# Optimization experiments

Measured on AMD Instinct MI355X. Metric: run time of the kernel, lower is better.

Reference implementation:

```python
import jax, jax.numpy as jnp
import numpy as np

D_MODEL = 1024
NUM_HEADS = 16
D_K = D_MODEL // NUM_HEADS
R = 8
ALPHA = 16
SCALING = ALPHA / R


def _lora_linear(x, W, b, A, Bm):
    # base: x @ W.T + b ; lora: (x @ A.T) @ Bm.T * scaling
    base = jnp.einsum('btd,od->bto', x, W) + b
    lora = jnp.einsum('btr,or->bto', jnp.einsum('btd,rd->btr', x, A), Bm) * SCALING
    return base + lora


def setup_inputs() -> dict:
    key = jax.random.key(0)
    ks = jax.random.split(key, 20)
    B, T = 2, 2048
    inp = {
        'q': jax.random.normal(ks[0], (B, T, D_MODEL), jnp.float32),
        'k': jax.random.normal(ks[1], (B, T, D_MODEL), jnp.float32),
        'v': jax.random.normal(ks[2], (B, T, D_MODEL), jnp.float32),
        'mask': jnp.ones((1, 1, T, T), jnp.int32),
    }
    i = 3
    for name in ('q', 'k', 'v'):
        inp[f'W{name}'] = jax.random.normal(ks[i], (D_MODEL, D_MODEL), jnp.float32) * 0.02; i += 1
        inp[f'b{name}'] = jnp.zeros((D_MODEL,), jnp.float32)
        inp[f'A{name}'] = jax.random.normal(ks[i], (R, D_MODEL), jnp.float32) * 0.01; i += 1
        inp[f'B{name}'] = jax.random.normal(ks[i], (D_MODEL, R), jnp.float32) * 0.01; i += 1
    inp['Wo'] = jax.random.normal(ks[i], (D_MODEL, D_MODEL), jnp.float32) * 0.02
    inp['bo'] = jnp.zeros((D_MODEL,), jnp.float32)
    return inp


def reference(q, k, v, mask, Wq, bq, Aq, Bq, Wk, bk, Ak, Bk, Wv, bv, Av, Bv, Wo, bo):
    B, Tq, _ = q.shape
    Tk = k.shape[1]
    Q = _lora_linear(q, Wq, bq, Aq, Bq).reshape(B, Tq, NUM_HEADS, D_K).transpose(0, 2, 1, 3)
    K = _lora_linear(k, Wk, bk, Ak, Bk).reshape(B, Tk, NUM_HEADS, D_K).transpose(0, 2, 1, 3)
    V = _lora_linear(v, Wv, bv, Av, Bv).reshape(B, Tk, NUM_HEADS, D_K).transpose(0, 2, 1, 3)
    scores = jnp.einsum('bhqd,bhkd->bhqk', Q, K) / jnp.sqrt(jnp.float32(D_K))
    scores = jnp.where(mask == 0, jnp.float32(-1e9), scores)
    attn = jax.nn.softmax(scores, axis=-1)
    out = jnp.einsum('bhqk,bhkd->bhqd', attn, V)
    out = out.transpose(0, 2, 1, 3).reshape(B, Tq, D_MODEL)
    return jnp.einsum('btd,od->bto', out, Wo) + bo
```

## Files before the change

kernel.cpp:

```cpp
#include <hip/hip_runtime.h>
#include <stdint.h>

typedef unsigned short u16;
typedef __attribute__((ext_vector_type(4))) float f32x4;
typedef __attribute__((ext_vector_type(4))) uint32_t u32x4;
typedef __attribute__((ext_vector_type(8))) __bf16 bf16x8;

#if __has_builtin(__builtin_amdgcn_exp2f)
#define EXP2(x) __builtin_amdgcn_exp2f(x)
#else
#define EXP2(x) exp2f(x)
#endif

static __device__ __forceinline__ u16 f2bf(float f) {
    union { float f; uint32_t i; } v; v.f = f;
    return (u16)((v.i + 0x7FFFu + ((v.i >> 16) & 1u)) >> 16);
}
static __device__ __forceinline__ uint32_t cvtpk(float lo, float hi) {
    uint32_t r;
    asm("v_cvt_pk_bf16_f32 %0, %1, %2" : "=v"(r) : "v"(lo), "v"(hi));
    return r;
}

static __device__ __forceinline__ void gl2lds16(const u16* g, u16* lds) {
    __builtin_amdgcn_global_load_lds(
        (const __attribute__((address_space(1))) void*)g,
        (__attribute__((address_space(3))) void*)lds, 16, 0, 0);
}

struct PrepArgs {
    const float* csrc[7]; u16* cdst[7];
    const float* A[3]; u16* apk[3];
    const int* mask; int* flags;
};

__global__ __launch_bounds__(256)
void prep_kernel(PrepArgs a) {
    const int bid = blockIdx.x;
    const int tid = threadIdx.x;

    if (bid < 1024) {
        int arr, boff;
        if (bid < 768) { arr = bid >> 8; boff = bid & 255; }
        else { int b2 = bid - 768; arr = 3 + (b2 >> 6); boff = b2 & 63; }
        const float* s = a.csrc[arr] + (size_t)boff * 16384;
        u16* d = a.cdst[arr] + (size_t)boff * 16384;
#pragma unroll
        for (int i = 0; i < 8; ++i) {
            int c = tid + i * 256;
            float4 f0 = *(const float4*)(s + c * 8);
            float4 f1 = *(const float4*)(s + c * 8 + 4);
            u16 o[8];
            o[0] = f2bf(f0.x); o[1] = f2bf(f0.y); o[2] = f2bf(f0.z); o[3] = f2bf(f0.w);
            o[4] = f2bf(f1.x); o[5] = f2bf(f1.y); o[6] = f2bf(f1.z); o[7] = f2bf(f1.w);
            *(uint4*)(d + c * 8) = *(const uint4*)o;
        }
    } else if (bid < 1536) {
        const int b3 = bid - 1024;
        const int qb = b3 & 15, kt = b3 >> 4;
        int ok = 1;
#pragma unroll
        for (int i = 0; i < 8; ++i) {
            int c = tid + i * 256;
            int row = c >> 4, cg = c & 15;
            int4 m4 = *(const int4*)&a.mask[(size_t)(qb * 128 + row) * 2048 + kt * 64 + cg * 4];
            ok &= (m4.x != 0) & (m4.y != 0) & (m4.z != 0) & (m4.w != 0);
        }
        int wall = __all(ok) ? 1 : 0;
        __shared__ int red[4];
        if ((tid & 63) == 0) red[tid >> 6] = wall;
        __syncthreads();
        if (tid == 0) a.flags[qb * 32 + kt] = red[0] & red[1] & red[2] & red[3];
    } else {
        const int z = bid - 1536;
        const float* Az = a.A[z];
        u16* dp = a.apk[z];
#pragma unroll
        for (int i = 0; i < 8; ++i) {
            int pos = tid + i * 256;
            int lane2 = pos & 63;
            int l15_ = lane2 & 15, l4_ = lane2 >> 4;
            int kbkk = pos >> 6;
            int kcol = (kbkk >> 1) * 64 + (kbkk & 1) * 32 + l4_ * 8;
            u16 ob[8] = {0, 0, 0, 0, 0, 0, 0, 0};
            if (l15_ < 8) {
                float4 f0 = *(const float4*)&Az[(size_t)l15_ * 1024 + kcol];
                float4 f1 = *(const float4*)&Az[(size_t)l15_ * 1024 + kcol + 4];
                ob[0] = f2bf(f0.x); ob[1] = f2bf(f0.y); ob[2] = f2bf(f0.z); ob[3] = f2bf(f0.w);
                ob[4] = f2bf(f1.x); ob[5] = f2bf(f1.y); ob[6] = f2bf(f1.z); ob[7] = f2bf(f1.w);
            }
            *(uint4*)&dp[(size_t)pos * 8] = *(const uint4*)ob;
        }
    }
}

struct GemmPtrs { const u16* X; const u16* W; const float* bias; const u16* Ap; const float* Bm; void* out; int transT; float oscale; };
struct GemmArgs { GemmPtrs p[3]; };

#define LST 136
#define LTT 72

template <int WMT, int WNT, int LORA>
__global__ __launch_bounds__(256, 2)
void gemm_kernel(GemmArgs args) {
    constexpr int BM = WMT * 32, BN = WNT * 32;
    constexpr int MBLK = 4096 / BM;
    constexpr int IPA = BM / 32;
    constexpr int IPB = BN / 32;
    __shared__ alignas(16) u16 smem[(BM + BN) * 64];
    u16* As = smem;
    u16* Bs = smem + BM * 64;

    const GemmPtrs gp = args.p[blockIdx.z];
    const int tid = threadIdx.x;
    const int lane = tid & 63, wave = tid >> 6;
    const int wm = wave >> 1, wn = wave & 1;
    const int l15 = lane & 15, l4 = lane >> 4;
    const int id = blockIdx.x;
    const int m0 = (id % MBLK) * BM, n0 = (id / MBLK) * BN;

    const int srow = lane >> 3;
    const int scol = ((lane & 7) ^ srow) * 8;
    const u16* gA[IPA];
    const u16* gB[IPB];
#pragma unroll
    for (int i = 0; i < IPA; ++i) {
        int q = wave * IPA + i;
        gA[i] = gp.X + (size_t)(m0 + q * 8 + srow) * 1024 + scol;
    }
#pragma unroll
    for (int i = 0; i < IPB; ++i) {
        int q = wave * IPB + i;
        gB[i] = gp.W + (size_t)(n0 + q * 8 + srow) * 1024 + scol;
    }

    const f32x4 fz = {0.f, 0.f, 0.f, 0.f};
    f32x4 acc[WMT][WNT];
#pragma unroll
    for (int i = 0; i < WMT; ++i)
#pragma unroll
        for (int j = 0; j < WNT; ++j) acc[i][j] = fz;
    f32x4 acc_xa[WMT];
    if constexpr (LORA) {
#pragma unroll
        for (int i = 0; i < WMT; ++i) acc_xa[i] = fz;
    }

    const int sw = l15 & 7;
    for (int kb = 0; kb < 16; ++kb) {
        __syncthreads();
#pragma unroll
        for (int i = 0; i < IPA; ++i)
            gl2lds16(gA[i] + kb * 64, &As[(wave * IPA + i) * 512]);
#pragma unroll
        for (int i = 0; i < IPB; ++i)
            gl2lds16(gB[i] + kb * 64, &Bs[(wave * IPB + i) * 512]);
        __syncthreads();
#pragma unroll
        for (int kk2 = 0; kk2 < 2; ++kk2) {
            bf16x8 af[WMT], bfr[WNT];
#pragma unroll
            for (int mt = 0; mt < WMT; ++mt) {
                int x = wm * (WMT * 16) + mt * 16 + l15;
                af[mt] = *(const bf16x8*)&As[x * 64 + (((kk2 * 4 + l4) ^ sw) * 8)];
            }
#pragma unroll
            for (int nt = 0; nt < WNT; ++nt) {
                int y = wn * (WNT * 16) + nt * 16 + l15;
                bfr[nt] = *(const bf16x8*)&Bs[y * 64 + (((kk2 * 4 + l4) ^ sw) * 8)];
            }
#pragma unroll
            for (int mt = 0; mt < WMT; ++mt)
#pragma unroll
                for (int nt = 0; nt < WNT; ++nt)
                    acc[mt][nt] = __builtin_amdgcn_mfma_f32_16x16x32_bf16(af[mt], bfr[nt], acc[mt][nt], 0, 0, 0);
            if constexpr (LORA) {
                bf16x8 abf = *(const bf16x8*)&gp.Ap[(size_t)((kb * 2 + kk2) * 64 + lane) * 8];
#pragma unroll
                for (int mt = 0; mt < WMT; ++mt)
                    acc_xa[mt] = __builtin_amdgcn_mfma_f32_16x16x32_bf16(af[mt], abf, acc_xa[mt], 0, 0, 0);
            }
        }
    }

    if constexpr (LORA) {
        __syncthreads();
        float* XAs = (float*)smem;
        float* Bms = (float*)(smem + BM * 64);
        if (wn == 0 && l15 < 8) {
#pragma unroll
            for (int mt = 0; mt < WMT; ++mt)
#pragma unroll
                for (int r = 0; r < 4; ++r)
                    XAs[(wm * 64 + mt * 16 + l4 * 4 + r) * 8 + l15] = acc_xa[mt][r];
        }
        if (tid < 128) {
            *(float4*)&Bms[tid * 8]     = *(const float4*)&gp.Bm[(size_t)(n0 + tid) * 8];
            *(float4*)&Bms[tid * 8 + 4] = *(const float4*)&gp.Bm[(size_t)(n0 + tid) * 8 + 4];
        }
        __syncthreads();
        const float osc = gp.oscale;
        float bmv[WNT][8], bsv[WNT];
#pragma unroll
        for (int nt = 0; nt < WNT; ++nt) {
            int nloc = wn * 64 + nt * 16 + l15;
            bsv[nt] = gp.bias[n0 + nloc];
#pragma unroll
            for (int q8 = 0; q8 < 8; ++q8) bmv[nt][q8] = Bms[nloc * 8 + q8];
        }
#pragma unroll
        for (int mt = 0; mt < WMT; ++mt)
#pragma unroll
            for (int r = 0; r < 4; ++r) {
                int mloc = wm * 64 + mt * 16 + l4 * 4 + r;
                float xa8[8];
                *(float4*)&xa8[0] = *(const float4*)&XAs[mloc * 8];
                *(float4*)&xa8[4] = *(const float4*)&XAs[mloc * 8 + 4];
#pragma unroll
                for (int nt = 0; nt < WNT; ++nt) {
                    float lora = 0.f;
#pragma unroll
                    for (int q8 = 0; q8 < 8; ++q8) lora += xa8[q8] * bmv[nt][q8];
                    acc[mt][nt][r] = (acc[mt][nt][r] + bsv[nt] + 2.0f * lora) * osc;
                }
            }
        __syncthreads();

        u16* outp = (u16*)gp.out;
        const int bb = m0 >> 11;
        if (gp.transT) {
            u16* Lst = smem;
#pragma unroll
            for (int ch = 0; ch < 2; ++ch) {
#pragma unroll
                for (int mt2 = 0; mt2 < 2; ++mt2) {
                    int mt = ch * 2 + mt2;
#pragma unroll
                    for (int nt = 0; nt < WNT; ++nt)
#pragma unroll
                        for (int r = 0; r < 4; ++r)
                            Lst[(wn * 64 + nt * 16 + l15) * LTT + wm * 32 + mt2 * 16 + l4 * 4 + r] =
                                f2bf(acc[mt][nt][r]);
                }
                __syncthreads();
#pragma unroll
                for (int j = 0; j < 4; ++j) {
                    int w = tid + j * 256;
                    int nl = w >> 3, seg = w & 7;
                    uint4 val = *(const uint4*)&Lst[nl * LTT + seg * 8];
                    int n = n0 + nl, hh = n >> 6, dd = n & 63;
                    int c0 = seg * 8;
                    int gm = m0 + (c0 >> 5) * 64 + ch * 32 + (c0 & 31);
                    int t = gm & 2047;
                    *(uint4*)&outp[(((size_t)(bb * 16 + hh)) * 64 + dd) * 2048 + t] = val;
                }
                __syncthreads();
            }
        } else {
            u16* Ls = smem;
#pragma unroll
            for (int ch = 0; ch < 2; ++ch) {
#pragma unroll
                for (int mt2 = 0; mt2 < 2; ++mt2) {
                    int mt = ch * 2 + mt2;
#pragma unroll
                    for (int nt = 0; nt < WNT; ++nt)
#pragma unroll
                        for (int r = 0; r < 4; ++r)
                            Ls[(wm * 32 + mt2 * 16 + l4 * 4 + r) * LST + wn * 64 + nt * 16 + l15] =
                                f2bf(acc[mt][nt][r]);
                }
                __syncthreads();
#pragma unroll
                for (int j = 0; j < 4; ++j) {
                    int w = tid + j * 256;
                    int lrow = w >> 4, seg = w & 15;
                    uint4 val = *(const uint4*)&Ls[lrow * LST + seg * 8];
                    int gm = m0 + (lrow >> 5) * 64 + ch * 32 + (lrow & 31);
                    int t = gm & 2047;
                    int n = n0 + seg * 8, hh = n >> 6, dd = n & 63;
                    *(uint4*)&outp[(((size_t)(bb * 16 + hh)) * 2048 + t) * 64 + dd] = val;
                }
                __syncthreads();
            }
        }
    } else {
        float* outp = (float*)gp.out;
#pragma unroll
        for (int mt = 0; mt < WMT; ++mt)
#pragma unroll
            for (int r = 0; r < 4; ++r) {
                int m = m0 + wm * (WMT * 16) + mt * 16 + l4 * 4 + r;
#pragma unroll
                for (int nt = 0; nt < WNT; ++nt) {
                    int n = n0 + wn * (WNT * 16) + nt * 16 + l15;
                    outp[(size_t)m * 1024 + n] = acc[mt][nt][r] + gp.bias[n];
                }
            }
    }
}


__global__ __launch_bounds__(256, 4)
void attn_kernel(const u16* __restrict__ QKV, const int* __restrict__ mask,
                 const int* __restrict__ flags, u16* __restrict__ Xo) {
    const int qb = blockIdx.x >> 5;
    const int bh = blockIdx.x & 31;
    const int b = bh >> 4, h = bh & 15;
    const int tid = threadIdx.x;
    const int lane = tid & 63, wave = tid >> 6;
    const int l15 = lane & 15, l4 = lane >> 4;

    __shared__ alignas(16) u16 Ks[2][64 * 64];
    __shared__ alignas(16) u16 Vts[2][64 * 64];

    const size_t plane = (size_t)2 * 16 * 2048 * 64;
    const u16* Qg = QKV + (size_t)(b * 16 + h) * 2048 * 64;
    const u16* Kg = Qg + plane;
    const u16* Vg = Kg + plane;

    const int srow = lane >> 3;
    const int scol = ((lane & 7) ^ srow) * 8;

    const u16* kbase[2];
    const u16* vbase[2];
#pragma unroll
    for (int i = 0; i < 2; ++i) {
        int qq = wave * 2 + i;
        int kc = 16 * (qq & 1) + 8 * (srow >> 2) + 4 * ((qq >> 1) & 1) + (srow & 3) + 32 * (qq >> 2);
        kbase[i] = Kg + (size_t)kc * 64 + scol;
        vbase[i] = Vg + (size_t)(qq * 8 + srow) * 2048 + scol;
    }

    bf16x8 qa[2];
#pragma unroll
    for (int kk2 = 0; kk2 < 2; ++kk2)
        qa[kk2] = *(const bf16x8*)&Qg[(size_t)(qb * 64 + wave * 16 + l15) * 64 + kk2 * 32 + l4 * 8];

    const f32x4 fz = {0.f, 0.f, 0.f, 0.f};
    f32x4 accO[4];
#pragma unroll
    for (int dt = 0; dt < 4; ++dt) accO[dt] = fz;
    float lsum = 0.f;

#pragma unroll
    for (int i = 0; i < 2; ++i) {
        int qq = wave * 2 + i;
        gl2lds16(kbase[i], &Ks[0][qq * 512]);
        gl2lds16(vbase[i], &Vts[0][qq * 512]);
    }
    __syncthreads();

    for (int kt = 0; kt < 32; ++kt) {
        const u16* Kc = &Ks[kt & 1][0];
        const u16* Vc = &Vts[kt & 1][0];

        if (kt < 31) {
            u16* Kn = &Ks[(kt + 1) & 1][0];
            u16* Vn = &Vts[(kt + 1) & 1][0];
#pragma unroll
            for (int i = 0; i < 2; ++i) {
                int qq = wave * 2 + i;
                gl2lds16(kbase[i] + (size_t)(kt + 1) * 4096, &Kn[qq * 512]);
                gl2lds16(vbase[i] + (size_t)(kt + 1) * 64, &Vn[qq * 512]);
            }
        }

        f32x4 accS[4];
#pragma unroll
        for (int j = 0; j < 4; ++j) accS[j] = fz;
#pragma unroll
        for (int kk2 = 0; kk2 < 2; ++kk2) {
            bf16x8 kf[4];
#pragma unroll
            for (int j = 0; j < 4; ++j)
                kf[j] = *(const bf16x8*)&Kc[(j * 16 + l15) * 64 + (((kk2 * 4 + l4) ^ (l15 & 7)) * 8)];
            __builtin_amdgcn_s_setprio(1);
#pragma unroll
            for (int j = 0; j < 4; ++j)
                accS[j] = __builtin_amdgcn_mfma_f32_16x16x32_bf16(kf[j], qa[kk2], accS[j], 0, 0, 0);
            __builtin_amdgcn_s_setprio(0);
        }

        if (flags[(qb >> 1) * 32 + kt] == 0) {
            int qrow = qb * 64 + wave * 16 + l15;
#pragma unroll
            for (int j = 0; j < 4; ++j)
#pragma unroll
                for (int r = 0; r < 4; ++r) {
                    int kcol = kt * 64 + 8 * l4 + 4 * (j & 1) + r + 32 * (j >> 1);
                    if (mask[(size_t)qrow * 2048 + kcol] == 0) accS[j][r] = -1e9f;
                }
        }

        float part0 = 0.f, part1 = 0.f;
#pragma unroll
        for (int j = 0; j < 4; ++j)
#pragma unroll
            for (int r = 0; r < 4; ++r) {
                float p = EXP2(accS[j][r]);
                accS[j][r] = p;
                if (j & 1) part1 += p; else part0 += p;
            }
        lsum += part0 + part1;

        u32x4 paw0, paw1;
        paw0[0] = cvtpk(accS[0][0], accS[0][1]); paw0[1] = cvtpk(accS[0][2], accS[0][3]);
        paw0[2] = cvtpk(accS[1][0], accS[1][1]); paw0[3] = cvtpk(accS[1][2], accS[1][3]);
        paw1[0] = cvtpk(accS[2][0], accS[2][1]); paw1[1] = cvtpk(accS[2][2], accS[2][3]);
        paw1[2] = cvtpk(accS[3][0], accS[3][1]); paw1[3] = cvtpk(accS[3][2], accS[3][3]);
        bf16x8 pa[2];
        pa[0] = __builtin_bit_cast(bf16x8, paw0);
        pa[1] = __builtin_bit_cast(bf16x8, paw1);

#pragma unroll
        for (int kk2 = 0; kk2 < 2; ++kk2) {
            bf16x8 vf[4];
#pragma unroll
            for (int dt = 0; dt < 4; ++dt)
                vf[dt] = *(const bf16x8*)&Vc[(dt * 16 + l15) * 64 + (((kk2 * 4 + l4) ^ (l15 & 7)) * 8)];
            __builtin_amdgcn_s_setprio(1);
#pragma unroll
            for (int dt = 0; dt < 4; ++dt)
                accO[dt] = __builtin_amdgcn_mfma_f32_16x16x32_bf16(pa[kk2], vf[dt], accO[dt], 0, 0, 0);
            __builtin_amdgcn_s_setprio(0);
        }

        __syncthreads();
    }

    float tot = lsum;
    tot += __shfl_xor(tot, 16, 64);
    tot += __shfl_xor(tot, 32, 64);
    float inv[4];
#pragma unroll
    for (int r = 0; r < 4; ++r) inv[r] = 1.0f / __shfl(tot, l4 * 4 + r, 64);

    u16* Es = &Ks[0][0];
#pragma unroll
    for (int dt = 0; dt < 4; ++dt)
#pragma unroll
        for (int r = 0; r < 4; ++r) {
            int prow = wave * 16 + l4 * 4 + r;
            Es[prow * 64 + (((dt * 2 + (l15 >> 3)) ^ (prow & 7)) * 8) + (l15 & 7)] =
                f2bf(accO[dt][r] * inv[r]);
        }
    __syncthreads();
#pragma unroll
    for (int j = 0; j < 2; ++j) {
        int w = tid + j * 256;
        int row = w >> 3, seg = w & 7;
        uint4 val = *(const uint4*)&Es[row * 64 + ((seg ^ (row & 7)) * 8)];
        int t = qb * 64 + row;
        *(uint4*)&Xo[((size_t)(b * 2048 + t)) * 1024 + h * 64 + seg * 8] = val;
    }
}

extern "C" void kernel_launch(void* const* d_in, const int* in_sizes, int n_in,
                              void* d_out, int out_size, void* d_ws, size_t ws_size,
                              hipStream_t stream) {
    const float* q    = (const float*)d_in[0];
    const float* k    = (const float*)d_in[1];
    const float* v    = (const float*)d_in[2];
    const int*   mask = (const int*)d_in[3];
    const float* Wq = (const float*)d_in[4];
    const float* bq = (const float*)d_in[5];
    const float* Aq = (const float*)d_in[6];
    const float* Bq = (const float*)d_in[7];
    const float* Wk = (const float*)d_in[8];
    const float* bk = (const float*)d_in[9];
    const float* Ak = (const float*)d_in[10];
    const float* Bk = (const float*)d_in[11];
    const float* Wv = (const float*)d_in[12];
    const float* bv = (const float*)d_in[13];
    const float* Av = (const float*)d_in[14];
    const float* Bv = (const float*)d_in[15];
    const float* Wo = (const float*)d_in[16];
    const float* bo = (const float*)d_in[17];

    char* ws = (char*)d_ws;
    u16*   QKV   = (u16*)ws;
    u16*   qb16  = (u16*)(ws + 25165824);
    u16*   kb16  = (u16*)(ws + 33554432);
    u16*   vb16  = (u16*)(ws + 41943040);
    u16*   Wqb   = (u16*)(ws + 50331648);
    u16*   Wkb   = (u16*)(ws + 52428800);
    u16*   Wvb   = (u16*)(ws + 54525952);
    u16*   Wob   = (u16*)(ws + 56623104);
    u16*   Apk   = (u16*)(ws + 58720256);
    int*   flags = (int*)(ws + 59113472);
    u16*   Xbuf  = qb16;

    PrepArgs pa;
    pa.csrc[0] = q;  pa.csrc[1] = k;  pa.csrc[2] = v;
    pa.csrc[3] = Wq; pa.csrc[4] = Wk; pa.csrc[5] = Wv; pa.csrc[6] = Wo;
    pa.cdst[0] = qb16; pa.cdst[1] = kb16; pa.cdst[2] = vb16;
    pa.cdst[3] = Wqb;  pa.cdst[4] = Wkb;  pa.cdst[5] = Wvb; pa.cdst[6] = Wob;
    pa.A[0] = Aq; pa.A[1] = Ak; pa.A[2] = Av;
    pa.apk[0] = Apk; pa.apk[1] = Apk + 16384; pa.apk[2] = Apk + 32768;
    pa.mask = mask; pa.flags = flags;
    prep_kernel<<<dim3(1539), dim3(256), 0, stream>>>(pa);

    const float QSCALE = 0.1803368801f;
    GemmArgs g1;
    g1.p[0] = GemmPtrs{qb16, Wqb, bq, Apk,         Bq, (void*)QKV,             0, QSCALE};
    g1.p[1] = GemmPtrs{kb16, Wkb, bk, Apk + 16384, Bk, (void*)(QKV + 4194304), 0, 1.0f};
    g1.p[2] = GemmPtrs{vb16, Wvb, bv, Apk + 32768, Bv, (void*)(QKV + 8388608), 1, 1.0f};
    gemm_kernel<4, 4, 1><<<dim3(256, 1, 3), dim3(256), 0, stream>>>(g1);

    attn_kernel<<<dim3(1024), dim3(256), 0, stream>>>(QKV, mask, flags, Xbuf);

    GemmArgs g2;
    g2.p[0] = GemmPtrs{Xbuf, Wob, bo, nullptr, nullptr, d_out, 0, 1.0f};
    g2.p[1] = g2.p[0];
    g2.p[2] = g2.p[0];
    gemm_kernel<2, 4, 0><<<dim3(512, 1, 1), dim3(256), 0, stream>>>(g2);
}
```

Measured before the change: 255.4 us.

## Double-buffer LDS tiles in GEMM K-loop and prefetch LoRA A fragments

Splits shared memory into two stages so the next K-tile is copied from global memory into LDS while MFMAs run on the current tile. This removes one barrier per iteration. The LoRA A fragments are also loaded one iteration ahead in registers. The cost is twice the shared memory and extra registers, which may reduce occupancy.

```diff
diff --git a/kernel.cpp b/kernel.cpp
--- a/kernel.cpp
+++ b/kernel.cpp
@@ -107,9 +107,7 @@
     constexpr int MBLK = 4096 / BM;
     constexpr int IPA = BM / 32;
     constexpr int IPB = BN / 32;
-    __shared__ alignas(16) u16 smem[(BM + BN) * 64];
-    u16* As = smem;
-    u16* Bs = smem + BM * 64;
+    __shared__ alignas(16) u16 smem[2][(BM + BN) * 64];
 
     const GemmPtrs gp = args.p[blockIdx.z];
     const int tid = threadIdx.x;
@@ -141,21 +139,42 @@
 #pragma unroll
         for (int j = 0; j < WNT; ++j) acc[i][j] = fz;
     f32x4 acc_xa[WMT];
+    bf16x8 abf[2], abf_n[2];
     if constexpr (LORA) {
 #pragma unroll
         for (int i = 0; i < WMT; ++i) acc_xa[i] = fz;
-    }
+        abf[0] = *(const bf16x8*)&gp.Ap[(size_t)(0 * 64 + lane) * 8];
+        abf[1] = *(const bf16x8*)&gp.Ap[(size_t)(1 * 64 + lane) * 8];
+    }
+
+#pragma unroll
+    for (int i = 0; i < IPA; ++i)
+        gl2lds16(gA[i], &smem[0][(wave * IPA + i) * 512]);
+#pragma unroll
+    for (int i = 0; i < IPB; ++i)
+        gl2lds16(gB[i], &smem[0][BM * 64 + (wave * IPB + i) * 512]);
+    __syncthreads();
 
     const int sw = l15 & 7;
     for (int kb = 0; kb < 16; ++kb) {
-        __syncthreads();
-#pragma unroll
-        for (int i = 0; i < IPA; ++i)
-            gl2lds16(gA[i] + kb * 64, &As[(wave * IPA + i) * 512]);
-#pragma unroll
-        for (int i = 0; i < IPB; ++i)
-            gl2lds16(gB[i] + kb * 64, &Bs[(wave * IPB + i) * 512]);
-        __syncthreads();
+        const u16* As = &smem[kb & 1][0];
+        const u16* Bs = &smem[kb & 1][BM * 64];
+
+        if (kb < 15) {
+            if constexpr (LORA) {
+                abf_n[0] = *(const bf16x8*)&gp.Ap[(size_t)(((kb + 1) * 2 + 0) * 64 + lane) * 8];
+                abf_n[1] = *(const bf16x8*)&gp.Ap[(size_t)(((kb + 1) * 2 + 1) * 64 + lane) * 8];
+            }
+            u16* An = &smem[(kb + 1) & 1][0];
+            u16* Bn = &smem[(kb + 1) & 1][BM * 64];
+#pragma unroll
+            for (int i = 0; i < IPA; ++i)
+                gl2lds16(gA[i] + (kb + 1) * 64, &An[(wave * IPA + i) * 512]);
+#pragma unroll
+            for (int i = 0; i < IPB; ++i)
+                gl2lds16(gB[i] + (kb + 1) * 64, &Bn[(wave * IPB + i) * 512]);
+        }
+
 #pragma unroll
         for (int kk2 = 0; kk2 < 2; ++kk2) {
             bf16x8 af[WMT], bfr[WNT];
@@ -175,18 +194,21 @@
                 for (int nt = 0; nt < WNT; ++nt)
                     acc[mt][nt] = __builtin_amdgcn_mfma_f32_16x16x32_bf16(af[mt], bfr[nt], acc[mt][nt], 0, 0, 0);
             if constexpr (LORA) {
-                bf16x8 abf = *(const bf16x8*)&gp.Ap[(size_t)((kb * 2 + kk2) * 64 + lane) * 8];
 #pragma unroll
                 for (int mt = 0; mt < WMT; ++mt)
-                    acc_xa[mt] = __builtin_amdgcn_mfma_f32_16x16x32_bf16(af[mt], abf, acc_xa[mt], 0, 0, 0);
-            }
-        }
+                    acc_xa[mt] = __builtin_amdgcn_mfma_f32_16x16x32_bf16(af[mt], abf[kk2], acc_xa[mt], 0, 0, 0);
+            }
+        }
+        if constexpr (LORA) {
+            if (kb < 15) { abf[0] = abf_n[0]; abf[1] = abf_n[1]; }
+        }
+
+        __syncthreads();
     }
 
     if constexpr (LORA) {
-        __syncthreads();
-        float* XAs = (float*)smem;
-        float* Bms = (float*)(smem + BM * 64);
+        float* XAs = (float*)&smem[0][0];
+        float* Bms = (float*)&smem[0][BM * 64];
         if (wn == 0 && l15 < 8) {
 #pragma unroll
             for (int mt = 0; mt < WMT; ++mt)
@@ -229,7 +251,7 @@
         u16* outp = (u16*)gp.out;
         const int bb = m0 >> 11;
         if (gp.transT) {
-            u16* Lst = smem;
+            u16* Lst = &smem[0][0];
 #pragma unroll
             for (int ch = 0; ch < 2; ++ch) {
 #pragma unroll
@@ -257,7 +279,7 @@
                 __syncthreads();
             }
         } else {
-            u16* Ls = smem;
+            u16* Ls = &smem[0][0];
 #pragma unroll
             for (int ch = 0; ch < 2; ++ch) {
 #pragma unroll
```

Measured after the change: 245.0 us. 4.1% less time.
